# Performance work log

Hardware: AMD Instinct MI355X
Metric: run time of the kernel (lower is better)

Reference implementation:

```python
import math
import jax, jax.numpy as jnp
import numpy as np

LM_DAMPING = 1e-3
MOTION_LAMBDA = 1.0
LM_ITERS = (2, 3, 4)


def _skew(w):  # (B,3) -> (B,3,3)
    z = jnp.zeros_like(w[:, 0])
    return jnp.stack([z, -w[:, 2], w[:, 1],
                      w[:, 2], z, -w[:, 0],
                      -w[:, 1], w[:, 0], z], axis=-1).reshape(-1, 3, 3)


def _se3_exp(xi):  # (B,6) -> (B,4,4)
    t, w = xi[:, :3], xi[:, 3:]
    theta = jnp.clip(jnp.linalg.norm(w, axis=-1, keepdims=True), 1e-8, None)  # (B,1)
    K = _skew(w / theta)
    eye = jnp.eye(3, dtype=xi.dtype)
    st = jnp.sin(theta)[:, :, None]          # (B,1,1)
    ct = (1.0 - jnp.cos(theta))[:, :, None]
    KK = K @ K
    R = eye + st * K + ct * KK
    th = jnp.clip(theta[:, :, None], 1e-8, None)
    V = eye + (ct / th) * K + (1.0 - st / th) * KK
    t_out = (V @ t[..., None])[..., 0]
    B = xi.shape[0]
    T = jnp.tile(jnp.eye(4, dtype=xi.dtype)[None], (B, 1, 1))
    T = T.at[:, :3, :3].set(R).at[:, :3, 3].set(t_out)
    return T


def _se3_log(T):  # (B,4,4) -> (B,6)
    R, t = T[:, :3, :3], T[:, :3, 3]
    cos_a = (R[:, 0, 0] + R[:, 1, 1] + R[:, 2, 2] - 1.0) / 2.0
    theta = jnp.arccos(jnp.clip(cos_a, -1.0 + 1e-7, 1.0 - 1e-7))
    small = jnp.abs(theta) < 1e-6
    th = jnp.clip(theta, 1e-8, None)
    w = jnp.stack([R[:, 2, 1] - R[:, 1, 2],
                   R[:, 0, 2] - R[:, 2, 0],
                   R[:, 1, 0] - R[:, 0, 1]], axis=-1)
    w = w / (2.0 * jnp.clip(jnp.sin(th), 1e-8, None))[:, None] * th[:, None]
    w = jnp.where(small[:, None], 0.0, w)
    return jnp.concatenate([t, w], axis=-1)


def _sample_one(feat, gx, gy):
    # feat (C,H,W); gx,gy (P,) normalized in [-1,1]; align_corners=False, border padding
    C, H, W = feat.shape
    x = jnp.clip(((gx + 1.0) * W - 1.0) / 2.0, 0.0, W - 1)
    y = jnp.clip(((gy + 1.0) * H - 1.0) / 2.0, 0.0, H - 1)
    x0 = jnp.floor(x); y0 = jnp.floor(y)
    x1 = jnp.minimum(x0 + 1.0, W - 1); y1 = jnp.minimum(y0 + 1.0, H - 1)
    wx = x - x0; wy = y - y0
    x0i, x1i = x0.astype(jnp.int32), x1.astype(jnp.int32)
    y0i, y1i = y0.astype(jnp.int32), y1.astype(jnp.int32)
    f00 = feat[:, y0i, x0i]; f01 = feat[:, y0i, x1i]
    f10 = feat[:, y1i, x0i]; f11 = feat[:, y1i, x1i]
    return (f00 * (1 - wx) * (1 - wy) + f01 * wx * (1 - wy)
            + f10 * (1 - wx) * wy + f11 * wx * wy)  # (C,P)

_sample = jax.vmap(_sample_one, in_axes=(0, 0, 0))


def _generate_hypotheses(T_pred, key):
    rng = jnp.arange(-11.0, 13.0, 2.0, dtype=jnp.float32)  # 12 values
    pg, yg = jnp.meshgrid(rng, rng, indexing='ij')
    pitch = pg.reshape(-1) * (math.pi / 180.0)
    yaw = yg.reshape(-1) * (math.pi / 180.0)
    M = pitch.shape[0]  # 144
    t_noise = jax.random.normal(key, (M, 3), dtype=jnp.float32) * 1.0  # translation_std
    xi = jnp.stack([t_noise[:, 0], t_noise[:, 1], t_noise[:, 2],
                    jnp.zeros(M, jnp.float32), pitch, yaw], axis=-1)
    dT = _se3_exp(xi)  # (M,4,4)
    return jnp.einsum('mij,bjk->bmik', dT, T_pred)  # (B,M,4,4)


def _residuals(T, q_feat, r_feat, q_unc, geo, K, level):
    # T (B,M,4,4); fallback path evaluates only first min(M,16) hypotheses
    B, M = T.shape[:2]
    _, C, H, W = q_feat.shape
    scale = 1.0 / (4.0 / 2 ** level)
    Ks = jnp.concatenate([K[:, :2] * scale, K[:, 2:]], axis=1)
    M16 = min(M, 16)
    Tm = T[:, :M16]  # (B,16,4,4)
    N = geo.shape[1]
    pts_h = jnp.concatenate([geo, jnp.ones((B, N, 1), geo.dtype)], axis=-1)  # (B,N,4)
    pts_cam = jnp.einsum('bmij,bnj->bmni', Tm[:, :, :3, :], pts_h)  # (B,16,N,3)
    z = jnp.clip(pts_cam[..., 2:3], 1e-6, None)
    xy = pts_cam[..., :2] / z
    fx = Ks[:, 0, 0][:, None, None]; fy = Ks[:, 1, 1][:, None, None]
    cx = Ks[:, 0, 2][:, None, None]; cy = Ks[:, 1, 2][:, None, None]
    u = fx * xy[..., 0] + cx
    v = fy * xy[..., 1] + cy
    gx = (2.0 * u / max(W - 1, 1) - 1.0).reshape(B, M16 * N)
    gy = (2.0 * v / max(H - 1, 1) - 1.0).reshape(B, M16 * N)
    qs = _sample(q_feat, gx, gy).reshape(B, C, M16, N)
    rs = _sample(r_feat, gx, gy).reshape(B, C, M16, N)
    diff2 = (qs - rs) ** 2
    unc = _sample(q_unc, gx, gy).reshape(B, 1, M16, N)
    res = (diff2 * unc).sum(axis=1).mean(axis=-1)  # (B,16)
    return jnp.zeros((B, M), T.dtype).at[:, :M16].set(res)


def reference(T_pred, geo_anchors, intrinsics, q0, q1, q2, r0, r1, r2, u0, u1, u2):
    key = jax.random.key(42)
    B = T_pred.shape[0]
    T_cur = _generate_hypotheses(T_pred, jax.random.fold_in(key, 0))
    M = T_cur.shape[1]
    q_feats = (q0, q1, q2); r_feats = (r0, r1, r2); uncs = (u0, u1, u2)
    costs = jnp.zeros((B, M), T_pred.dtype)
    for level, n_iters in enumerate(LM_ITERS):
        for it in range(n_iters):
            res = _residuals(T_cur, q_feats[level], r_feats[level], uncs[level],
                             geo_anchors, intrinsics, level)
            damping = LM_DAMPING * 0.5 ** level
            noise = jax.random.normal(jax.random.fold_in(key, 100 + level * 10 + it),
                                      (B, M, 6), dtype=T_pred.dtype)
            step = -damping * res[..., None] * noise * 0.01
            delta = _se3_exp(step.reshape(B * M, 6)).reshape(B, M, 4, 4)
            T_cur = delta @ T_cur
            costs = res
    # motion-constrained selection: C_total = C_photo + lambda * ||log(T_ref T_pred^-1)||
    T_rel = T_cur @ jnp.linalg.inv(T_pred)[:, None]
    geod = jnp.linalg.norm(_se3_log(T_rel.reshape(B * M, 4, 4)), axis=-1).reshape(B, M)
    total = costs + MOTION_LAMBDA * geod
    idx = jnp.argmin(total, axis=1)
    T_best = jnp.take_along_axis(T_cur, idx[:, None, None, None], axis=1)[:, 0]
    return T_best, costs


def setup_inputs() -> dict:
    key = jax.random.key(0)
    ks = jax.random.split(key, 16)
    B, N = 8, 500
    # valid SE(3) predicted poses (small perturbation of identity)
    T_pred = _se3_exp(jax.random.normal(ks[0], (B, 6), jnp.float32) * 0.1)
    # 3D anchors in front of the camera (z ~ 6)
    geo = jax.random.uniform(ks[1], (B, N, 3), jnp.float32, -2.0, 2.0)
    geo = geo.at[..., 2].add(6.0)
    K = jnp.tile(jnp.array([[200.0, 0.0, 128.0],
                            [0.0, 200.0, 96.0],
                            [0.0, 0.0, 1.0]], jnp.float32)[None], (B, 1, 1))
    shapes_f = [(B, 128, 48, 64), (B, 64, 96, 128), (B, 32, 192, 256)]
    q = [jax.random.normal(ks[2 + i], s, jnp.float32) for i, s in enumerate(shapes_f)]
    r = [jax.random.normal(ks[5 + i], s, jnp.float32) for i, s in enumerate(shapes_f)]
    u = [jax.random.uniform(ks[8 + i], (s[0], 1, s[2], s[3]), jnp.float32)
         for i, s in enumerate(shapes_f)]
    return {"T_pred": T_pred, "geo_anchors": geo, "intrinsics": K,
            "q0": q[0], "q1": q[1], "q2": q[2],
            "r0": r[0], "r1": r[1], "r2": r[2],
            "u0": u[0], "u1": u[1], "u2": u[2]}
```

## Files before the change

### kernel.cpp

```cpp
#include <hip/hip_runtime.h>
#include <stdint.h>
#include <math.h>

#define JAX_PARTITIONABLE 1

#define NB 8
#define NM 144
#define NM16 16
#define NPTS 500
#define GP 16

__host__ __device__ __forceinline__ uint32_t rotl32(uint32_t x, int r) {
    return (x << r) | (x >> (32 - r));
}

__host__ __device__ inline void threefry2x32(uint32_t k0, uint32_t k1,
                                             uint32_t x0, uint32_t x1,
                                             uint32_t& o0, uint32_t& o1) {
    uint32_t ks2 = k0 ^ k1 ^ 0x1BD11BDAu;
    x0 += k0; x1 += k1;
    const int RA[4] = {13, 15, 26, 6};
    const int RB[4] = {17, 29, 16, 24};
#define R4(ROT) { x0 += x1; x1 = rotl32(x1, ROT[0]); x1 ^= x0; \
                  x0 += x1; x1 = rotl32(x1, ROT[1]); x1 ^= x0; \
                  x0 += x1; x1 = rotl32(x1, ROT[2]); x1 ^= x0; \
                  x0 += x1; x1 = rotl32(x1, ROT[3]); x1 ^= x0; }
    R4(RA); x0 += k1;  x1 += ks2 + 1u;
    R4(RB); x0 += ks2; x1 += k0 + 2u;
    R4(RA); x0 += k0;  x1 += k1 + 3u;
    R4(RB); x0 += k1;  x1 += ks2 + 4u;
    R4(RA); x0 += ks2; x1 += k0 + 5u;
#undef R4
    o0 = x0; o1 = x1;
}

__device__ __forceinline__ float erfinv32(float x) {
    float w = -log1pf(-x * x);
    float p;
    if (w < 5.0f) {
        w = w - 2.5f;
        p = 2.81022636e-08f;
        p = fmaf(p, w, 3.43273939e-07f);
        p = fmaf(p, w, -3.5233877e-06f);
// ... 114 lines not shown
    double t1 = V[3] * tx + V[4] * ty + V[5] * tz;
    double t2 = V[6] * tx + V[7] * ty + V[8] * tz;
    T[0] = R[0]; T[1] = R[1]; T[2] = R[2];  T[3] = t0;
    T[4] = R[3]; T[5] = R[4]; T[6] = R[5];  T[7] = t1;
    T[8] = R[6]; T[9] = R[7]; T[10] = R[8]; T[11] = t2;
}

__device__ inline void compose44d(const double dT[12], const double P[16], double Tn[16]) {
    for (int i = 0; i < 3; i++)
        for (int j = 0; j < 4; j++)
            Tn[i * 4 + j] = dT[i * 4 + 0] * P[0 + j] + dT[i * 4 + 1] * P[4 + j] +
                            dT[i * 4 + 2] * P[8 + j] + dT[i * 4 + 3] * P[12 + j];
    Tn[12] = 0.0; Tn[13] = 0.0; Tn[14] = 0.0; Tn[15] = 1.0;
}

__device__ inline void make_hypothesis_d(int m, const double* P, uint32_t hk0, uint32_t hk1,
                                         double Tn[16]) {
    float tn[3];
    for (int c = 0; c < 3; c++)
        tn[c] = jax_normal(hk0, hk1, (uint32_t)(m * 3 + c), 216u);
    int gi = m / 12, gj = m % 12;
    const float d2r = (float)(M_PI / 180.0);
    float pf = (float)(2 * gi - 11) * d2r;
    float yf = (float)(2 * gj - 11) * d2r;
    double xi[6] = {(double)tn[0], (double)tn[1], (double)tn[2], 0.0,
                    (double)pf, (double)yf};
    double dT[12];
    se3_exp6d(xi, dT);
    compose44d(dT, P, Tn);
}

struct IterKeys { uint32_t k0[9]; uint32_t k1[9]; float damping[9]; };

template <int C, int H, int W, int GRP>
__device__ void gram_body_v(const float* __restrict__ q, const float* __restrict__ r,
                            const float* __restrict__ u, float* __restrict__ G,
                            float* part, int blk) {
    constexpr int HW = H * W;
    constexpr int PT = 256 / GRP;
    constexpr int PPB = PT * 4;
    constexpr int TPB = HW / PPB;
    constexpr int CPG = C / GRP;
    const int b = blk / TPB;
    const int tile = blk % TPB;
    const int tid = threadIdx.x;
    const int g = tid / PT;
    const int p = tid % PT;
    const int px0 = tile * PPB + p * 4;
    const int y = px0 / W;
    const int x0 = px0 - y * W;
    const int y1 = (y + 1 < H) ? y + 1 : H - 1;
    const bool edge = (x0 + 4 >= W);

    const int rb0 = y * W + x0;
    const int rb1 = y1 * W + x0;
    const float* qp = q + ((size_t)b * C + (size_t)g * CPG) * HW;
    const float* rp = r + ((size_t)b * C + (size_t)g * CPG) * HW;

    float acc[4][10];
#pragma unroll
    for (int j = 0; j < 4; j++)
#pragma unroll
        for (int i = 0; i < 10; i++) acc[j][i] = 0.0f;

#pragma unroll 2
    for (int c = 0; c < CPG; c++) {
        float4 a0 = *(const float4*)(qp + rb0);
        float4 a1 = *(const float4*)(qp + rb1);
        float4 b0 = *(const float4*)(rp + rb0);
        float4 b1 = *(const float4*)(rp + rb1);
        qp += HW; rp += HW;
        float e0[5], e1[5];
        e0[0] = a0.x - b0.x; e0[1] = a0.y - b0.y; e0[2] = a0.z - b0.z; e0[3] = a0.w - b0.w;
        e1[0] = a1.x - b1.x; e1[1] = a1.y - b1.y; e1[2] = a1.z - b1.z; e1[3] = a1.w - b1.w;
        float d0n = __shfl_down(e0[0], 1, 64);
        float d1n = __shfl_down(e1[0], 1, 64);
        e0[4] = edge ? e0[3] : d0n;
        e1[4] = edge ? e1[3] : d1n;
#pragma unroll
        for (int j = 0; j < 4; j++) {
            float d00 = e0[j], d01 = e0[j + 1];
            float d10 = e1[j], d11 = e1[j + 1];
            acc[j][0] = fmaf(d00, d00, acc[j][0]);
            acc[j][1] = fmaf(d00, d01, acc[j][1]);
            acc[j][2] = fmaf(d00, d10, acc[j][2]);
            acc[j][3] = fmaf(d00, d11, acc[j][3]);
            acc[j][4] = fmaf(d01, d01, acc[j][4]);
            acc[j][5] = fmaf(d01, d10, acc[j][5]);
            acc[j][6] = fmaf(d01, d11, acc[j][6]);
            acc[j][7] = fmaf(d10, d10, acc[j][7]);
            acc[j][8] = fmaf(d10, d11, acc[j][8]);
            acc[j][9] = fmaf(d11, d11, acc[j][9]);
        }
    }
    if (GRP > 1) {
        if (g > 0) {
            float* pp = part + (size_t)(g - 1) * 40 * PT;
#pragma unroll
            for (int j = 0; j < 4; j++)
#pragma unroll
                for (int i = 0; i < 10; i++)
                    pp[(j * 10 + i) * PT + p] = acc[j][i];
        }
        __syncthreads();
        if (g == 0) {
            for (int gg = 1; gg < GRP; gg++) {
                const float* pp = part + (size_t)(gg - 1) * 40 * PT;
#pragma unroll
                for (int j = 0; j < 4; j++)
#pragma unroll
                    for (int i = 0; i < 10; i++)
                        acc[j][i] += pp[(j * 10 + i) * PT + p];
            }
        }
    }
    if (g == 0) {
        const float* ub = u + (size_t)b * HW;
        float4 u0 = *(const float4*)(ub + rb0);
        float4 u1 = *(const float4*)(ub + rb1);
        float w0[5], w1[5];
        w0[0] = u0.x; w0[1] = u0.y; w0[2] = u0.z; w0[3] = u0.w;
        w1[0] = u1.x; w1[1] = u1.y; w1[2] = u1.z; w1[3] = u1.w;
        float u0n = __shfl_down(u0.x, 1, 64);
        float u1n = __shfl_down(u1.x, 1, 64);
        w0[4] = edge ? w0[3] : u0n;
        w1[4] = edge ? w1[3] : u1n;
#pragma unroll
        for (int j = 0; j < 4; j++) {
            size_t base = ((size_t)b * HW + px0 + j) * GP;
            float4 g0v = {acc[j][0], acc[j][1], acc[j][2], acc[j][3]};
            float4 g1v = {acc[j][4], acc[j][5], acc[j][6], acc[j][7]};
            float4 g2v = {acc[j][8], acc[j][9], w0[j], w0[j + 1]};
            float4 g3v = {w1[j], w1[j + 1], 0.0f, 0.0f};
            *(float4*)(G + base + 0)  = g0v;
            *(float4*)(G + base + 4)  = g1v;
            *(float4*)(G + base + 8)  = g2v;
            *(float4*)(G + base + 12) = g3v;
        }
    }
}

#define VBLK0 96
#define VBLK1 192
#define VBLK2 384

__global__ __launch_bounds__(256) void gram_fused_kernel(
    const float* __restrict__ q0, const float* __restrict__ r0, const float* __restrict__ u0,
    float* __restrict__ G0,
    const float* __restrict__ q1, const float* __restrict__ r1, const float* __restrict__ u1,
    float* __restrict__ G1,
    const float* __restrict__ q2, const float* __restrict__ r2, const float* __restrict__ u2,
    float* __restrict__ G2) {
    __shared__ float part[3 * 40 * 64];
    const int blk = blockIdx.x;
    if (blk < VBLK0)
        gram_body_v<128, 48, 64, 4>(q0, r0, u0, G0, part, blk);
    else if (blk < VBLK0 + VBLK1)
        gram_body_v<64, 96, 128, 2>(q1, r1, u1, G1, part, blk - VBLK0);
    else
        gram_body_v<32, 192, 256, 1>(q2, r2, u2, G2, part, blk - VBLK0 - VBLK1);
}

template <int H, int W>
__device__ void run_level_gram(const float* __restrict__ Gb,
                               float fx, float fy, float cx, float cy,
                               const float* geoS, float* Tsh, float* red, float* resS,
                               float* stepS, float* out, int b, int m,
                               const IterKeys& iks, int firstIter, int niter) {
    const int tid = threadIdx.x;
    for (int it = 0; it < niter; it++) {
        const int iter = firstIter + it;
        float acc = 0.0f;
        if (tid < NPTS) {
            float px = geoS[tid * 3], py = geoS[tid * 3 + 1], pz = geoS[tid * 3 + 2];
            float X = Tsh[0] * px + Tsh[1] * py + Tsh[2]  * pz + Tsh[3];
            float Y = Tsh[4] * px + Tsh[5] * py + Tsh[6]  * pz + Tsh[7];
            float Z = Tsh[8] * px + Tsh[9] * py + Tsh[10] * pz + Tsh[11];
            float z = fmaxf(Z, 1e-6f);
            float uu = fx * (X / z) + cx;
            float vv = fy * (Y / z) + cy;
            float gx = 2.0f * uu / (float)(W - 1) - 1.0f;
            float gy = 2.0f * vv / (float)(H - 1) - 1.0f;
            float x = fminf(fmaxf(((gx + 1.0f) * (float)W - 1.0f) * 0.5f, 0.0f), (float)(W - 1));
            float y = fminf(fmaxf(((gy + 1.0f) * (float)H - 1.0f) * 0.5f, 0.0f), (float)(H - 1));
            float x0f = floorf(x), y0f = floorf(y);
            float wx = x - x0f, wy = y - y0f;
            int x0i = (int)x0f, y0i = (int)y0f;
            int i00 = y0i * W + x0i;
            float w00 = (1.0f - wx) * (1.0f - wy), w01 = wx * (1.0f - wy);
            float w10 = (1.0f - wx) * wy,          w11 = wx * wy;
            const float* Gp = Gb + (size_t)i00 * GP;
            float4 g0 = *(const float4*)(Gp + 0);
            float4 g1 = *(const float4*)(Gp + 4);
            float4 g2 = *(const float4*)(Gp + 8);
            float4 g3 = *(const float4*)(Gp + 12);
            float uval = w00 * g2.z + w01 * g2.w + w10 * g3.x + w11 * g3.y;
            float val = w00 * w00 * g0.x + w01 * w01 * g1.x +
                        w10 * w10 * g1.w + w11 * w11 * g2.y +
                        2.0f * (w00 * w01 * g0.y + w00 * w10 * g0.z + w00 * w11 * g0.w +
                                w01 * w10 * g1.y + w01 * w11 * g1.z + w10 * w11 * g2.x);
            acc = uval * val;
        }
        float v = acc;
        for (int off = 32; off > 0; off >>= 1) v += __shfl_down(v, off, 64);
        if ((tid & 63) == 0) red[tid >> 6] = v;
        __syncthreads();
        if (tid == 0) {
            float s = 0.0f;
            for (int w = 0; w < 8; w++) s += red[w];
            float res = s / 500.0f;
            *resS = res;
            if (iter == 8) out[128 + b * NM + m] = res;
        }
        __syncthreads();
        if (tid < 6) {
            uint32_t fi = (uint32_t)((b * NM + m) * 6 + tid);
            float nz = jax_normal(iks.k0[iter], iks.k1[iter], fi, 3456u);
            stepS[tid] = (((-iks.damping[iter]) * (*resS)) * nz) * 0.01f;
        }
        __syncthreads();
        if (tid == 0) {
            float xi[6];
            for (int j = 0; j < 6; j++) xi[j] = stepS[j];
            float dT[12];
            se3_exp6(xi, dT);
            float Told[16];
            for (int k = 0; k < 16; k++) Told[k] = Tsh[k];
            float Tn[16];
            compose44(dT, Told, Tn);
            for (int k = 0; k < 16; k++) Tsh[k] = Tn[k];
        }
        __syncthreads();
    }
}

__global__ __launch_bounds__(512) void evolve_kernel_gram(
    const float* __restrict__ T_pred, const float* __restrict__ geo,
    const float* __restrict__ Kmat,
    const float* __restrict__ G0, const float* __restrict__ G1, const float* __restrict__ G2,
    float* __restrict__ Tws, float* __restrict__ out,
    uint32_t hk0, uint32_t hk1, IterKeys iks) {
    const int bm = blockIdx.x;
    const int b = bm & 7;
    const int m = bm >> 3;
    const int tid = threadIdx.x;

    __shared__ float Tsh[16];
    __shared__ float geoS[NPTS * 3];
    __shared__ float red[8];
    __shared__ float resS;
    __shared__ float stepS[6];

    for (int i = tid; i < NPTS * 3; i += 512) geoS[i] = geo[b * NPTS * 3 + i];

    if (tid == 0) {
        float P[16];
        for (int k = 0; k < 16; k++) P[k] = T_pred[b * 16 + k];
        float Tn[16];
        make_hypothesis(m, P, hk0, hk1, Tn);
        for (int k = 0; k < 16; k++) Tsh[k] = Tn[k];
    }
    __syncthreads();

    float K00 = Kmat[b * 9 + 0], K02 = Kmat[b * 9 + 2];
    float K11 = Kmat[b * 9 + 4], K12 = Kmat[b * 9 + 5];

    run_level_gram<48, 64>(G0 + (size_t)b * 48 * 64 * GP,
                           K00 * 0.25f, K11 * 0.25f, K02 * 0.25f, K12 * 0.25f,
                           geoS, Tsh, red, &resS, stepS, out, b, m, iks, 0, 2);
    run_level_gram<96, 128>(G1 + (size_t)b * 96 * 128 * GP,
                            K00 * 0.5f, K11 * 0.5f, K02 * 0.5f, K12 * 0.5f,
                            geoS, Tsh, red, &resS, stepS, out, b, m, iks, 2, 3);
    run_level_gram<192, 256>(G2 + (size_t)b * 192 * 256 * GP,
                             K00, K11, K02, K12,
                             geoS, Tsh, red, &resS, stepS, out, b, m, iks, 5, 4);

    if (tid < 16) Tws[(size_t)(b * NM16 + m) * 16 + tid] = Tsh[tid];
}

template <int C, int H, int W>
__device__ void run_level_nchw(const float* __restrict__ qb, const float* __restrict__ rb,
                               const float* __restrict__ ub,
                               float fx, float fy, float cx, float cy,
                               const float* geoS, float* Tsh, float* red, float* resS,
                               float* stepS, float* out, int b, int m,
                               const IterKeys& iks, int firstIter, int niter) {
    const int tid = threadIdx.x;
    const int HW = H * W;
    for (int it = 0; it < niter; it++) {
        const int iter = firstIter + it;
        float acc = 0.0f;
        if (tid < NPTS) {
            float px = geoS[tid * 3], py = geoS[tid * 3 + 1], pz = geoS[tid * 3 + 2];
            float X = Tsh[0] * px + Tsh[1] * py + Tsh[2]  * pz + Tsh[3];
            float Y = Tsh[4] * px + Tsh[5] * py + Tsh[6]  * pz + Tsh[7];
            float Z = Tsh[8] * px + Tsh[9] * py + Tsh[10] * pz + Tsh[11];
            float z = fmaxf(Z, 1e-6f);
            float uu = fx * (X / z) + cx;
            float vv = fy * (Y / z) + cy;
            float gx = 2.0f * uu / (float)(W - 1) - 1.0f;
            float gy = 2.0f * vv / (float)(H - 1) - 1.0f;
            float x = fminf(fmaxf(((gx + 1.0f) * (float)W - 1.0f) * 0.5f, 0.0f), (float)(W - 1));
            float y = fminf(fmaxf(((gy + 1.0f) * (float)H - 1.0f) * 0.5f, 0.0f), (float)(H - 1));
            float x0f = floorf(x), y0f = floorf(y);
            float x1f = fminf(x0f + 1.0f, (float)(W - 1));
            float y1f = fminf(y0f + 1.0f, (float)(H - 1));
            float wx = x - x0f, wy = y - y0f;
            int x0i = (int)x0f, x1i = (int)x1f, y0i = (int)y0f, y1i = (int)y1f;
            int i00 = y0i * W + x0i, i01 = y0i * W + x1i;
            int i10 = y1i * W + x0i, i11 = y1i * W + x1i;
// ... 165 lines not shown
    const float* K      = (const float*)d_in[2];
    const float* q0 = (const float*)d_in[3];
    const float* q1 = (const float*)d_in[4];
    const float* q2 = (const float*)d_in[5];
    const float* r0 = (const float*)d_in[6];
    const float* r1 = (const float*)d_in[7];
    const float* r2 = (const float*)d_in[8];
    const float* u0 = (const float*)d_in[9];
    const float* u1 = (const float*)d_in[10];
    const float* u2 = (const float*)d_in[11];
    float* out = (float*)d_out;

    float* Tws = (float*)d_ws;
    const size_t nG0 = (size_t)NB * 48 * 64 * GP;
    const size_t nG1 = (size_t)NB * 96 * 128 * GP;
    const size_t nG2 = (size_t)NB * 192 * 256 * GP;
    float* G0 = Tws + 2048;
    float* G1 = G0 + nG0;
    float* G2 = G1 + nG1;
    const size_t need = (2048 + nG0 + nG1 + nG2) * sizeof(float);

    uint32_t hk0, hk1;
    threefry2x32(0u, 42u, 0u, 0u, hk0, hk1);
    IterKeys iks;
    const int seeds[9] = {100, 101, 110, 111, 112, 120, 121, 122, 123};
    const float damp[9] = {0.001f, 0.001f, 0.0005f, 0.0005f, 0.0005f,
                           0.00025f, 0.00025f, 0.00025f, 0.00025f};
    for (int i = 0; i < 9; i++) {
        threefry2x32(0u, 42u, 0u, (uint32_t)seeds[i], iks.k0[i], iks.k1[i]);
        iks.damping[i] = damp[i];
    }

    if (ws_size >= need) {
        gram_fused_kernel<<<dim3(VBLK0 + VBLK1 + VBLK2), dim3(256), 0, stream>>>(
            q0, r0, u0, G0, q1, r1, u1, G1, q2, r2, u2, G2);
        evolve_kernel_gram<<<dim3(NB * NM16), dim3(512), 0, stream>>>(
            T_pred, geo, K, G0, G1, G2, Tws, out, hk0, hk1, iks);
    } else {
        evolve_kernel_nchw<<<dim3(NB * NM16), dim3(512), 0, stream>>>(
            T_pred, geo, K, q0, q1, q2, r0, r1, r2, u0, u1, u2, Tws, out, hk0, hk1, iks);
    }
    finalize_kernel<<<dim3(NB), dim3(192), 0, stream>>>(T_pred, Tws, out, hk0, hk1);
}
```

Before: 256.9 us.

## Halve pixels per thread in gram kernel, swizzle blocks, precompute LM noise

The gram-precompute kernel now gives each thread 2 pixels instead of 4. This doubles the block count for more parallelism on the bandwidth-bound q/r reads, and a straddle path handles the neighbour pixel across wavefront boundaries. Block indices are remapped with an interleaving swizzle across the three pyramid levels. In the evolve kernel, the per-iteration normal noise and damping are precomputed into shared memory once, and the step reduction runs within one wavefront via shuffles, removing two barriers per iteration. The cost is narrower float2 loads and extra scalar loads for straddling lanes.

```diff
diff --git a/kernel.cpp b/kernel.cpp
--- a/kernel.cpp
+++ b/kernel.cpp
@@ -195,7 +195,7 @@
                             float* part, int blk) {
     constexpr int HW = H * W;
     constexpr int PT = 256 / GRP;
-    constexpr int PPB = PT * 4;
+    constexpr int PPB = PT * 2;
     constexpr int TPB = HW / PPB;
     constexpr int CPG = C / GRP;
     const int b = blk / TPB;
@@ -203,58 +203,68 @@
     const int tid = threadIdx.x;
     const int g = tid / PT;
     const int p = tid % PT;
-    const int px0 = tile * PPB + p * 4;
+    const int px0 = tile * PPB + p * 2;
     const int y = px0 / W;
     const int x0 = px0 - y * W;
     const int y1 = (y + 1 < H) ? y + 1 : H - 1;
-    const bool edge = (x0 + 4 >= W);
+    const bool edge = (x0 + 2 >= W);
+    const bool straddle = (!edge) && ((tid & 63) == 63);
 
     const int rb0 = y * W + x0;
     const int rb1 = y1 * W + x0;
     const float* qp = q + ((size_t)b * C + (size_t)g * CPG) * HW;
     const float* rp = r + ((size_t)b * C + (size_t)g * CPG) * HW;
 
-    float acc[4][10];
+    float acc[2][10];
 #pragma unroll
-    for (int j = 0; j < 4; j++)
+    for (int j = 0; j < 2; j++)
 #pragma unroll
         for (int i = 0; i < 10; i++) acc[j][i] = 0.0f;
 
 #pragma unroll 2
     for (int c = 0; c < CPG; c++) {
-        float4 a0 = *(const float4*)(qp + rb0);
-        float4 a1 = *(const float4*)(qp + rb1);
-        float4 b0 = *(const float4*)(rp + rb0);
-        float4 b1 = *(const float4*)(rp + rb1);
+        float2 a0 = *(const float2*)(qp + rb0);
+        float2 a1 = *(const float2*)(qp + rb1);
+        float2 b0 = *(const float2*)(rp + rb0);
+        float2 b1 = *(const float2*)(rp + rb1);
+        float s0 = 0.0f, s1 = 0.0f;
+        if (straddle) {
+            s0 = qp[rb0 + 2] - rp[rb0 + 2];
+            s1 = qp[rb1 + 2] - rp[rb1 + 2];
+        }
         qp += HW; rp += HW;
-        float e0[5], e1[5];
-        e0[0] = a0.x - b0.x; e0[1] = a0.y - b0.y; e0[2] = a0.z - b0.z; e0[3] = a0.w - b0.w;
-        e1[0] = a1.x - b1.x; e1[1] = a1.y - b1.y; e1[2] = a1.z - b1.z; e1[3] = a1.w - b1.w;
-        float d0n = __shfl_down(e0[0], 1, 64);
-        float d1n = __shfl_down(e1[0], 1, 64);
-        e0[4] = edge ? e0[3] : d0n;
-        e1[4] = edge ? e1[3] : d1n;
-#pragma unroll
-        for (int j = 0; j < 4; j++) {
-            float d00 = e0[j], d01 = e0[j + 1];
-            float d10 = e1[j], d11 = e1[j + 1];
-            acc[j][0] = fmaf(d00, d00, acc[j][0]);
-            acc[j][1] = fmaf(d00, d01, acc[j][1]);
-            acc[j][2] = fmaf(d00, d10, acc[j][2]);
-            acc[j][3] = fmaf(d00, d11, acc[j][3]);
-            acc[j][4] = fmaf(d01, d01, acc[j][4]);
-            acc[j][5] = fmaf(d01, d10, acc[j][5]);
-            acc[j][6] = fmaf(d01, d11, acc[j][6]);
-            acc[j][7] = fmaf(d10, d10, acc[j][7]);
-            acc[j][8] = fmaf(d10, d11, acc[j][8]);
-            acc[j][9] = fmaf(d11, d11, acc[j][9]);
-        }
+        float e00 = a0.x - b0.x, e01 = a0.y - b0.y;
+        float e10 = a1.x - b1.x, e11 = a1.y - b1.y;
+        float d0n = __shfl_down(e00, 1, 64);
+        float d1n = __shfl_down(e10, 1, 64);
+        float e02 = edge ? e01 : (straddle ? s0 : d0n);
+        float e12 = edge ? e11 : (straddle ? s1 : d1n);
+        acc[0][0] = fmaf(e00, e00, acc[0][0]);
+        acc[0][1] = fmaf(e00, e01, acc[0][1]);
+        acc[0][2] = fmaf(e00, e10, acc[0][2]);
+        acc[0][3] = fmaf(e00, e11, acc[0][3]);
+        acc[0][4] = fmaf(e01, e01, acc[0][4]);
+        acc[0][5] = fmaf(e01, e10, acc[0][5]);
+        acc[0][6] = fmaf(e01, e11, acc[0][6]);
+        acc[0][7] = fmaf(e10, e10, acc[0][7]);
+        acc[0][8] = fmaf(e10, e11, acc[0][8]);
+        acc[0][9] = fmaf(e11, e11, acc[0][9]);
+        acc[1][0] = fmaf(e01, e01, acc[1][0]);
+        acc[1][1] = fmaf(e01, e02, acc[1][1]);
+        acc[1][2] = fmaf(e01, e11, acc[1][2]);
+        acc[1][3] = fmaf(e01, e12, acc[1][3]);
+        acc[1][4] = fmaf(e02, e02, acc[1][4]);
+        acc[1][5] = fmaf(e02, e11, acc[1][5]);
+        acc[1][6] = fmaf(e02, e12, acc[1][6]);
+        acc[1][7] = fmaf(e11, e11, acc[1][7]);
+        acc[1][8] = fmaf(e11, e12, acc[1][8]);
+        acc[1][9] = fmaf(e12, e12, acc[1][9]);
     }
     if (GRP > 1) {
         if (g > 0) {
-            float* pp = part + (size_t)(g - 1) * 40 * PT;
+            float* pp = part + (size_t)(g - 1) * 20 * PT;
 #pragma unroll
-            for (int j = 0; j < 4; j++)
+            for (int j = 0; j < 2; j++)
 #pragma unroll
                 for (int i = 0; i < 10; i++)
                     pp[(j * 10 + i) * PT + p] = acc[j][i];
@@ -262,9 +272,9 @@
         __syncthreads();
         if (g == 0) {
             for (int gg = 1; gg < GRP; gg++) {
-                const float* pp = part + (size_t)(gg - 1) * 40 * PT;
+                const float* pp = part + (size_t)(gg - 1) * 20 * PT;
 #pragma unroll
-                for (int j = 0; j < 4; j++)
+                for (int j = 0; j < 2; j++)
 #pragma unroll
                     for (int i = 0; i < 10; i++)
                         acc[j][i] += pp[(j * 10 + i) * PT + p];
@@ -273,33 +283,45 @@
     }
     if (g == 0) {
         const float* ub = u + (size_t)b * HW;
-        float4 u0 = *(const float4*)(ub + rb0);
-        float4 u1 = *(const float4*)(ub + rb1);
-        float w0[5], w1[5];
-        w0[0] = u0.x; w0[1] = u0.y; w0[2] = u0.z; w0[3] = u0.w;
-        w1[0] = u1.x; w1[1] = u1.y; w1[2] = u1.z; w1[3] = u1.w;
+        float2 u0 = *(const float2*)(ub + rb0);
+        float2 u1 = *(const float2*)(ub + rb1);
+        float su0 = 0.0f, su1 = 0.0f;
+        if (straddle) { su0 = ub[rb0 + 2]; su1 = ub[rb1 + 2]; }
+        float w00 = u0.x, w01 = u0.y;
+        float w10 = u1.x, w11 = u1.y;
         float u0n = __shfl_down(u0.x, 1, 64);
         float u1n = __shfl_down(u1.x, 1, 64);
-        w0[4] = edge ? w0[3] : u0n;
-        w1[4] = edge ? w1[3] : u1n;
-#pragma unroll
-        for (int j = 0; j < 4; j++) {
-            size_t base = ((size_t)b * HW + px0 + j) * GP;
-            float4 g0v = {acc[j][0], acc[j][1], acc[j][2], acc[j][3]};
-            float4 g1v = {acc[j][4], acc[j][5], acc[j][6], acc[j][7]};
-            float4 g2v = {acc[j][8], acc[j][9], w0[j], w0[j + 1]};
-            float4 g3v = {w1[j], w1[j + 1], 0.0f, 0.0f};
+        float w02 = edge ? w01 : (straddle ? su0 : u0n);
+        float w12 = edge ? w11 : (straddle ? su1 : u1n);
+        {
+            size_t base = ((size_t)b * HW + px0) * GP;
+            float4 g0v = {acc[0][0], acc[0][1], acc[0][2], acc[0][3]};
+            float4 g1v = {acc[0][4], acc[0][5], acc[0][6], acc[0][7]};
+            float4 g2v = {acc[0][8], acc[0][9], w00, w01};
+            float4 g3v = {w10, w11, 0.0f, 0.0f};
             *(float4*)(G + base + 0)  = g0v;
             *(float4*)(G + base + 4)  = g1v;
             *(float4*)(G + base + 8)  = g2v;
             *(float4*)(G + base + 12) = g3v;
         }
-    }
-}
-
-#define VBLK0 96
-#define VBLK1 192
-#define VBLK2 384
+        {
+            size_t base = ((size_t)b * HW + px0 + 1) * GP;
+            float4 g0v = {acc[1][0], acc[1][1], acc[1][2], acc[1][3]};
+            float4 g1v = {acc[1][4], acc[1][5], acc[1][6], acc[1][7]};
+            float4 g2v = {acc[1][8], acc[1][9], w01, w02};
+            float4 g3v = {w11, w12, 0.0f, 0.0f};
+            *(float4*)(G + base + 0)  = g0v;
+            *(float4*)(G + base + 4)  = g1v;
+            *(float4*)(G + base + 8)  = g2v;
+            *(float4*)(G + base + 12) = g3v;
+        }
+    }
+}
+
+#define VBLK0 192
+#define VBLK1 384
+#define VBLK2 768
+#define VBLKT (VBLK0 + VBLK1 + VBLK2)
 
 __global__ __launch_bounds__(256) void gram_fused_kernel(
     const float* __restrict__ q0, const float* __restrict__ r0, const float* __restrict__ u0,
@@ -308,8 +330,8 @@
     float* __restrict__ G1,
     const float* __restrict__ q2, const float* __restrict__ r2, const float* __restrict__ u2,
     float* __restrict__ G2) {
-    __shared__ float part[3 * 40 * 64];
-    const int blk = blockIdx.x;
+    __shared__ float part[3 * 20 * 64];
+    const int blk = (blockIdx.x & 7) * (VBLKT / 8) + (blockIdx.x >> 3);
     if (blk < VBLK0)
         gram_body_v<128, 48, 64, 4>(q0, r0, u0, G0, part, blk);
     else if (blk < VBLK0 + VBLK1)
@@ -321,9 +343,9 @@
 template <int H, int W>
 __device__ void run_level_gram(const float* __restrict__ Gb,
                                float fx, float fy, float cx, float cy,
-                               const float* geoS, float* Tsh, float* red, float* resS,
-                               float* stepS, float* out, int b, int m,
-                               const IterKeys& iks, int firstIter, int niter) {
+                               const float* geoS, float* Tsh, float* red,
+                               const float* nzS, const float* damping,
+                               float* out, int b, int m, int firstIter, int niter) {
     const int tid = threadIdx.x;
     for (int it = 0; it < niter; it++) {
         const int iter = firstIter + it;
@@ -362,30 +384,26 @@
         for (int off = 32; off > 0; off >>= 1) v += __shfl_down(v, off, 64);
         if ((tid & 63) == 0) red[tid >> 6] = v;
         __syncthreads();
-        if (tid == 0) {
+        if (tid < 64) {
             float s = 0.0f;
             for (int w = 0; w < 8; w++) s += red[w];
             float res = s / 500.0f;
-            *resS = res;
-            if (iter == 8) out[128 + b * NM + m] = res;
-        }
-        __syncthreads();
-        if (tid < 6) {
-            uint32_t fi = (uint32_t)((b * NM + m) * 6 + tid);
-            float nz = jax_normal(iks.k0[iter], iks.k1[iter], fi, 3456u);
-            stepS[tid] = (((-iks.damping[iter]) * (*resS)) * nz) * 0.01f;
-        }
-        __syncthreads();
-        if (tid == 0) {
+            if (tid == 0 && iter == 8) out[128 + b * NM + m] = res;
+            float st = 0.0f;
+            if (tid < 6)
+                st = (((-damping[iter]) * res) * nzS[iter * 6 + tid]) * 0.01f;
             float xi[6];
-            for (int j = 0; j < 6; j++) xi[j] = stepS[j];
-            float dT[12];
-            se3_exp6(xi, dT);
-            float Told[16];
-            for (int k = 0; k < 16; k++) Told[k] = Tsh[k];
-            float Tn[16];
-            compose44(dT, Told, Tn);
-            for (int k = 0; k < 16; k++) Tsh[k] = Tn[k];
+#pragma unroll
+            for (int j = 0; j < 6; j++) xi[j] = __shfl(st, j, 64);
+            if (tid == 0) {
+                float dT[12];
+                se3_exp6(xi, dT);
+                float Told[16];
+                for (int k = 0; k < 16; k++) Told[k] = Tsh[k];
+                float Tn[16];
+                compose44(dT, Told, Tn);
+                for (int k = 0; k < 16; k++) Tsh[k] = Tn[k];
+            }
         }
         __syncthreads();
     }
@@ -405,12 +423,19 @@
     __shared__ float Tsh[16];
     __shared__ float geoS[NPTS * 3];
     __shared__ float red[8];
-    __shared__ float resS;
-    __shared__ float stepS[6];
+    __shared__ float nzS[54];
+    __shared__ float dampS[9];
 
     for (int i = tid; i < NPTS * 3; i += 512) geoS[i] = geo[b * NPTS * 3 + i];
 
-    if (tid == 0) {
+    if (tid < 54) {
+        int it9 = tid / 6, jj = tid % 6;
+        uint32_t fi = (uint32_t)((b * NM + m) * 6 + jj);
+        nzS[tid] = jax_normal(iks.k0[it9], iks.k1[it9], fi, 3456u);
+    }
+    if (tid >= 54 && tid < 63) dampS[tid - 54] = iks.damping[tid - 54];
+
+    if (tid == 64) {
         float P[16];
         for (int k = 0; k < 16; k++) P[k] = T_pred[b * 16 + k];
         float Tn[16];
@@ -424,13 +449,13 @@
 
     run_level_gram<48, 64>(G0 + (size_t)b * 48 * 64 * GP,
                            K00 * 0.25f, K11 * 0.25f, K02 * 0.25f, K12 * 0.25f,
-                           geoS, Tsh, red, &resS, stepS, out, b, m, iks, 0, 2);
+                           geoS, Tsh, red, nzS, dampS, out, b, m, 0, 2);
     run_level_gram<96, 128>(G1 + (size_t)b * 96 * 128 * GP,
                             K00 * 0.5f, K11 * 0.5f, K02 * 0.5f, K12 * 0.5f,
-                            geoS, Tsh, red, &resS, stepS, out, b, m, iks, 2, 3);
+                            geoS, Tsh, red, nzS, dampS, out, b, m, 2, 3);
     run_level_gram<192, 256>(G2 + (size_t)b * 192 * 256 * GP,
                              K00, K11, K02, K12,
-                             geoS, Tsh, red, &resS, stepS, out, b, m, iks, 5, 4);
+                             geoS, Tsh, red, nzS, dampS, out, b, m, 5, 4);
 
     if (tid < 16) Tws[(size_t)(b * NM16 + m) * 16 + tid] = Tsh[tid];
 }
@@ -664,7 +689,7 @@
     }
 
     if (ws_size >= need) {
-        gram_fused_kernel<<<dim3(VBLK0 + VBLK1 + VBLK2), dim3(256), 0, stream>>>(
+        gram_fused_kernel<<<dim3(VBLKT), dim3(256), 0, stream>>>(
             q0, r0, u0, G0, q1, r1, u1, G1, q2, r2, u2, G2);
         evolve_kernel_gram<<<dim3(NB * NM16), dim3(512), 0, stream>>>(
             T_pred, geo, K, G0, G1, G2, Tws, out, hk0, hk1, iks);
```

Result: slower. 267.3 us (+4.0%).

## Stage q/r feature rows in shared-memory slabs and precompute LM noise

Applied to the files above, without the earlier changes.

The gram kernel now assigns each block a band of four rows. For every channel it loads the rows plus one halo row into a double-buffered shared-memory slab, prefetched one channel ahead through registers, so the right-neighbour and lower-row values come from LDS rather than redundant global reads and shuffles. The evolve kernel precomputes all per-iteration Threefry noise and damping values into shared memory once, and collapses the per-iteration residual/step/update sequence into a single wavefront, removing two block barriers per LM iteration. The cost is two barriers per channel in the gram loop and extra LDS use, which may reduce occupancy.

```diff
diff --git a/kernel.cpp b/kernel.cpp
--- a/kernel.cpp
+++ b/kernel.cpp
@@ -189,30 +189,44 @@
 
 struct IterKeys { uint32_t k0[9]; uint32_t k1[9]; float damping[9]; };
 
+#define STF 2560
+
 template <int C, int H, int W, int GRP>
-__device__ void gram_body_v(const float* __restrict__ q, const float* __restrict__ r,
+__device__ void gram_body_s(const float* __restrict__ q, const float* __restrict__ r,
                             const float* __restrict__ u, float* __restrict__ G,
-                            float* part, int blk) {
+                            float* slab, float* part, int blk) {
     constexpr int HW = H * W;
+    constexpr int CPG = C / GRP;
+    constexpr int R = 4;
     constexpr int PT = 256 / GRP;
-    constexpr int PPB = PT * 4;
-    constexpr int TPB = HW / PPB;
-    constexpr int CPG = C / GRP;
+    constexpr int SPAN = (R + 1) * W;
+    constexpr int TPB = H / R;
+    constexpr int TPR = W / 4;
     const int b = blk / TPB;
     const int tile = blk % TPB;
+    const int y0 = tile * R;
     const int tid = threadIdx.x;
     const int g = tid / PT;
     const int p = tid % PT;
-    const int px0 = tile * PPB + p * 4;
-    const int y = px0 / W;
-    const int x0 = px0 - y * W;
-    const int y1 = (y + 1 < H) ? y + 1 : H - 1;
-    const bool edge = (x0 + 4 >= W);
-
-    const int rb0 = y * W + x0;
-    const int rb1 = y1 * W + x0;
-    const float* qp = q + ((size_t)b * C + (size_t)g * CPG) * HW;
-    const float* rp = r + ((size_t)b * C + (size_t)g * CPG) * HW;
+    const int row_l = p / TPR;
+    const int x0 = (p % TPR) * 4;
+
+    const float* ptrk[5];
+    int swk[5];
+#pragma unroll
+    for (int k = 0; k < 5; k++) {
+        int f = 2 * (tid + 256 * k);
+        swk[k] = f;
+        int arr = f / (GRP * SPAN);
+        int rem = f - arr * (GRP * SPAN);
+        int chl = rem / SPAN;
+        int rr  = rem - chl * SPAN;
+        int row = rr / W;
+        int x   = rr - row * W;
+        int gy  = (y0 + row < H) ? (y0 + row) : (H - 1);
+        const float* base = arr ? r : q;
+        ptrk[k] = base + ((size_t)b * C + (size_t)chl * CPG) * HW + (size_t)gy * W + x;
+    }
 
     float acc[4][10];
 #pragma unroll
@@ -220,36 +234,61 @@
 #pragma unroll
         for (int i = 0; i < 10; i++) acc[j][i] = 0.0f;
 
-#pragma unroll 2
-    for (int c = 0; c < CPG; c++) {
-        float4 a0 = *(const float4*)(qp + rb0);
-        float4 a1 = *(const float4*)(qp + rb1);
-        float4 b0 = *(const float4*)(rp + rb0);
-        float4 b1 = *(const float4*)(rp + rb1);
-        qp += HW; rp += HW;
+    float2 ld[5];
+#pragma unroll
+    for (int k = 0; k < 5; k++) { ld[k] = *(const float2*)ptrk[k]; ptrk[k] += HW; }
+#pragma unroll
+    for (int k = 0; k < 5; k++) *(float2*)&slab[swk[k]] = ld[k];
+#pragma unroll
+    for (int k = 0; k < 5; k++) { ld[k] = *(const float2*)ptrk[k]; ptrk[k] += HW; }
+    __syncthreads();
+
+    int cur = 0;
+    const int off0 = row_l * W + x0;
+    const int off1 = off0 + W;
+    const int t4 = (x0 + 4 < W) ? (x0 + 4) : (W - 1);
+    for (int j = 0; j < CPG; j++) {
+        const float* qs = slab + cur * STF + g * SPAN;
+        const float* rs = slab + cur * STF + (GRP + g) * SPAN;
+        float4 qa = *(const float4*)(qs + off0);
+        float4 qb = *(const float4*)(qs + off1);
+        float4 ra = *(const float4*)(rs + off0);
+        float4 rb = *(const float4*)(rs + off1);
+        float qa4 = qs[row_l * W + t4], qb4 = qs[row_l * W + W + t4];
+        float ra4 = rs[row_l * W + t4], rb4 = rs[row_l * W + W + t4];
         float e0[5], e1[5];
-        e0[0] = a0.x - b0.x; e0[1] = a0.y - b0.y; e0[2] = a0.z - b0.z; e0[3] = a0.w - b0.w;
-        e1[0] = a1.x - b1.x; e1[1] = a1.y - b1.y; e1[2] = a1.z - b1.z; e1[3] = a1.w - b1.w;
-        float d0n = __shfl_down(e0[0], 1, 64);
-        float d1n = __shfl_down(e1[0], 1, 64);
-        e0[4] = edge ? e0[3] : d0n;
-        e1[4] = edge ? e1[3] : d1n;
-#pragma unroll
-        for (int j = 0; j < 4; j++) {
-            float d00 = e0[j], d01 = e0[j + 1];
-            float d10 = e1[j], d11 = e1[j + 1];
-            acc[j][0] = fmaf(d00, d00, acc[j][0]);
-            acc[j][1] = fmaf(d00, d01, acc[j][1]);
-            acc[j][2] = fmaf(d00, d10, acc[j][2]);
-            acc[j][3] = fmaf(d00, d11, acc[j][3]);
-            acc[j][4] = fmaf(d01, d01, acc[j][4]);
-            acc[j][5] = fmaf(d01, d10, acc[j][5]);
-            acc[j][6] = fmaf(d01, d11, acc[j][6]);
-            acc[j][7] = fmaf(d10, d10, acc[j][7]);
-            acc[j][8] = fmaf(d10, d11, acc[j][8]);
-            acc[j][9] = fmaf(d11, d11, acc[j][9]);
-        }
-    }
+        e0[0] = qa.x - ra.x; e0[1] = qa.y - ra.y; e0[2] = qa.z - ra.z; e0[3] = qa.w - ra.w;
+        e0[4] = qa4 - ra4;
+        e1[0] = qb.x - rb.x; e1[1] = qb.y - rb.y; e1[2] = qb.z - rb.z; e1[3] = qb.w - rb.w;
+        e1[4] = qb4 - rb4;
+#pragma unroll
+        for (int jj = 0; jj < 4; jj++) {
+            float d00 = e0[jj], d01 = e0[jj + 1];
+            float d10 = e1[jj], d11 = e1[jj + 1];
+            acc[jj][0] = fmaf(d00, d00, acc[jj][0]);
+            acc[jj][1] = fmaf(d00, d01, acc[jj][1]);
+            acc[jj][2] = fmaf(d00, d10, acc[jj][2]);
+            acc[jj][3] = fmaf(d00, d11, acc[jj][3]);
+            acc[jj][4] = fmaf(d01, d01, acc[jj][4]);
+            acc[jj][5] = fmaf(d01, d10, acc[jj][5]);
+            acc[jj][6] = fmaf(d01, d11, acc[jj][6]);
+            acc[jj][7] = fmaf(d10, d10, acc[jj][7]);
+            acc[jj][8] = fmaf(d10, d11, acc[jj][8]);
+            acc[jj][9] = fmaf(d11, d11, acc[jj][9]);
+        }
+        __syncthreads();
+        if (j + 1 < CPG) {
+#pragma unroll
+            for (int k = 0; k < 5; k++) *(float2*)&slab[(cur ^ 1) * STF + swk[k]] = ld[k];
+            if (j + 2 < CPG) {
+#pragma unroll
+                for (int k = 0; k < 5; k++) { ld[k] = *(const float2*)ptrk[k]; ptrk[k] += HW; }
+            }
+        }
+        __syncthreads();
+        cur ^= 1;
+    }
+
     if (GRP > 1) {
         if (g > 0) {
             float* pp = part + (size_t)(g - 1) * 40 * PT;
@@ -271,17 +310,30 @@
             }
         }
     }
+
+#pragma unroll
+    for (int k = 0; k < 3; k++) {
+        int e2u = tid + 256 * k;
+        if (2 * e2u < SPAN) {
+            int f = 2 * e2u;
+            int row = f / W;
+            int x = f - row * W;
+            int gy = (y0 + row < H) ? (y0 + row) : (H - 1);
+            float2 v = *(const float2*)(u + (size_t)b * HW + (size_t)gy * W + x);
+            *(float2*)&slab[f] = v;
+        }
+    }
+    __syncthreads();
     if (g == 0) {
-        const float* ub = u + (size_t)b * HW;
-        float4 u0 = *(const float4*)(ub + rb0);
-        float4 u1 = *(const float4*)(ub + rb1);
         float w0[5], w1[5];
-        w0[0] = u0.x; w0[1] = u0.y; w0[2] = u0.z; w0[3] = u0.w;
-        w1[0] = u1.x; w1[1] = u1.y; w1[2] = u1.z; w1[3] = u1.w;
-        float u0n = __shfl_down(u0.x, 1, 64);
-        float u1n = __shfl_down(u1.x, 1, 64);
-        w0[4] = edge ? w0[3] : u0n;
-        w1[4] = edge ? w1[3] : u1n;
+#pragma unroll
+        for (int j = 0; j < 4; j++) {
+            w0[j] = slab[off0 + j];
+            w1[j] = slab[off1 + j];
+        }
+        w0[4] = slab[row_l * W + t4];
+        w1[4] = slab[row_l * W + W + t4];
+        const int px0 = (y0 + row_l) * W + x0;
 #pragma unroll
         for (int j = 0; j < 4; j++) {
             size_t base = ((size_t)b * HW + px0 + j) * GP;
@@ -297,9 +349,10 @@
     }
 }
 
-#define VBLK0 96
-#define VBLK1 192
-#define VBLK2 384
+#define SBLK0 96
+#define SBLK1 192
+#define SBLK2 384
+#define SBLKT (SBLK0 + SBLK1 + SBLK2)
 
 __global__ __launch_bounds__(256) void gram_fused_kernel(
     const float* __restrict__ q0, const float* __restrict__ r0, const float* __restrict__ u0,
@@ -308,22 +361,23 @@
     float* __restrict__ G1,
     const float* __restrict__ q2, const float* __restrict__ r2, const float* __restrict__ u2,
     float* __restrict__ G2) {
+    __shared__ float slab[2 * STF];
     __shared__ float part[3 * 40 * 64];
     const int blk = blockIdx.x;
-    if (blk < VBLK0)
-        gram_body_v<128, 48, 64, 4>(q0, r0, u0, G0, part, blk);
-    else if (blk < VBLK0 + VBLK1)
-        gram_body_v<64, 96, 128, 2>(q1, r1, u1, G1, part, blk - VBLK0);
+    if (blk < SBLK0)
+        gram_body_s<128, 48, 64, 4>(q0, r0, u0, G0, slab, part, blk);
+    else if (blk < SBLK0 + SBLK1)
+        gram_body_s<64, 96, 128, 2>(q1, r1, u1, G1, slab, part, blk - SBLK0);
     else
-        gram_body_v<32, 192, 256, 1>(q2, r2, u2, G2, part, blk - VBLK0 - VBLK1);
+        gram_body_s<32, 192, 256, 1>(q2, r2, u2, G2, slab, part, blk - SBLK0 - SBLK1);
 }
 
 template <int H, int W>
 __device__ void run_level_gram(const float* __restrict__ Gb,
                                float fx, float fy, float cx, float cy,
-                               const float* geoS, float* Tsh, float* red, float* resS,
-                               float* stepS, float* out, int b, int m,
-                               const IterKeys& iks, int firstIter, int niter) {
+                               const float* geoS, float* Tsh, float* red,
+                               const float* nzS, const float* damping,
+                               float* out, int b, int m, int firstIter, int niter) {
     const int tid = threadIdx.x;
     for (int it = 0; it < niter; it++) {
         const int iter = firstIter + it;
@@ -362,30 +416,26 @@
         for (int off = 32; off > 0; off >>= 1) v += __shfl_down(v, off, 64);
         if ((tid & 63) == 0) red[tid >> 6] = v;
         __syncthreads();
-        if (tid == 0) {
+        if (tid < 64) {
             float s = 0.0f;
             for (int w = 0; w < 8; w++) s += red[w];
             float res = s / 500.0f;
-            *resS = res;
-            if (iter == 8) out[128 + b * NM + m] = res;
-        }
-        __syncthreads();
-        if (tid < 6) {
-            uint32_t fi = (uint32_t)((b * NM + m) * 6 + tid);
-            float nz = jax_normal(iks.k0[iter], iks.k1[iter], fi, 3456u);
-            stepS[tid] = (((-iks.damping[iter]) * (*resS)) * nz) * 0.01f;
-        }
-        __syncthreads();
-        if (tid == 0) {
+            if (tid == 0 && iter == 8) out[128 + b * NM + m] = res;
+            float st = 0.0f;
+            if (tid < 6)
+                st = (((-damping[iter]) * res) * nzS[iter * 6 + tid]) * 0.01f;
             float xi[6];
-            for (int j = 0; j < 6; j++) xi[j] = stepS[j];
-            float dT[12];
-            se3_exp6(xi, dT);
-            float Told[16];
-            for (int k = 0; k < 16; k++) Told[k] = Tsh[k];
-            float Tn[16];
-            compose44(dT, Told, Tn);
-            for (int k = 0; k < 16; k++) Tsh[k] = Tn[k];
+#pragma unroll
+            for (int j = 0; j < 6; j++) xi[j] = __shfl(st, j, 64);
+            if (tid == 0) {
+                float dT[12];
+                se3_exp6(xi, dT);
+                float Told[16];
+                for (int k = 0; k < 16; k++) Told[k] = Tsh[k];
+                float Tn[16];
+                compose44(dT, Told, Tn);
+                for (int k = 0; k < 16; k++) Tsh[k] = Tn[k];
+            }
         }
         __syncthreads();
     }
@@ -405,12 +455,19 @@
     __shared__ float Tsh[16];
     __shared__ float geoS[NPTS * 3];
     __shared__ float red[8];
-    __shared__ float resS;
-    __shared__ float stepS[6];
+    __shared__ float nzS[54];
+    __shared__ float dampS[9];
 
     for (int i = tid; i < NPTS * 3; i += 512) geoS[i] = geo[b * NPTS * 3 + i];
 
-    if (tid == 0) {
+    if (tid < 54) {
+        int it9 = tid / 6, jj = tid % 6;
+        uint32_t fi = (uint32_t)((b * NM + m) * 6 + jj);
+        nzS[tid] = jax_normal(iks.k0[it9], iks.k1[it9], fi, 3456u);
+    }
+    if (tid >= 54 && tid < 63) dampS[tid - 54] = iks.damping[tid - 54];
+
+    if (tid == 64) {
         float P[16];
         for (int k = 0; k < 16; k++) P[k] = T_pred[b * 16 + k];
         float Tn[16];
@@ -424,13 +481,13 @@
 
     run_level_gram<48, 64>(G0 + (size_t)b * 48 * 64 * GP,
                            K00 * 0.25f, K11 * 0.25f, K02 * 0.25f, K12 * 0.25f,
-                           geoS, Tsh, red, &resS, stepS, out, b, m, iks, 0, 2);
+                           geoS, Tsh, red, nzS, dampS, out, b, m, 0, 2);
     run_level_gram<96, 128>(G1 + (size_t)b * 96 * 128 * GP,
                             K00 * 0.5f, K11 * 0.5f, K02 * 0.5f, K12 * 0.5f,
-                            geoS, Tsh, red, &resS, stepS, out, b, m, iks, 2, 3);
+                            geoS, Tsh, red, nzS, dampS, out, b, m, 2, 3);
     run_level_gram<192, 256>(G2 + (size_t)b * 192 * 256 * GP,
                              K00, K11, K02, K12,
-                             geoS, Tsh, red, &resS, stepS, out, b, m, iks, 5, 4);
+                             geoS, Tsh, red, nzS, dampS, out, b, m, 5, 4);
 
     if (tid < 16) Tws[(size_t)(b * NM16 + m) * 16 + tid] = Tsh[tid];
 }
@@ -664,7 +721,7 @@
     }
 
     if (ws_size >= need) {
-        gram_fused_kernel<<<dim3(VBLK0 + VBLK1 + VBLK2), dim3(256), 0, stream>>>(
+        gram_fused_kernel<<<dim3(SBLKT), dim3(256), 0, stream>>>(
             q0, r0, u0, G0, q1, r1, u1, G1, q2, r2, u2, G2);
         evolve_kernel_gram<<<dim3(NB * NM16), dim3(512), 0, stream>>>(
             T_pred, geo, K, G0, G1, G2, Tws, out, hk0, hk1, iks);
```

Result: no change. 252.1 us (-1.9%).

## Keep pose in registers per thread, precompute noise, use nontemporal loads

Applied to the files above, without the earlier changes.

The evolve kernel now keeps the 3x4 pose in registers of every thread. Each thread redundantly computes the residual sum, the SE(3) step and the pose update, so only one barrier per iteration remains instead of four. The per-iteration noise values and damping are precomputed into shared memory at kernel start, and the reduction buffer is double-buffered to avoid a write-after-read race. The gram kernel's feature loads switch to nontemporal loads to reduce cache pollution. The cost is redundant transcendental work across 512 threads and higher register pressure.

```diff
diff --git a/kernel.cpp b/kernel.cpp
--- a/kernel.cpp
+++ b/kernel.cpp
@@ -9,6 +9,12 @@
 #define NM16 16
 #define NPTS 500
 #define GP 16
+
+typedef float v4f __attribute__((ext_vector_type(4)));
+
+__device__ __forceinline__ v4f nt4(const float* p) {
+    return __builtin_nontemporal_load((const v4f*)p);
+}
 
 __host__ __device__ __forceinline__ uint32_t rotl32(uint32_t x, int r) {
     return (x << r) | (x >> (32 - r));
@@ -222,10 +228,10 @@
 
 #pragma unroll 2
     for (int c = 0; c < CPG; c++) {
-        float4 a0 = *(const float4*)(qp + rb0);
-        float4 a1 = *(const float4*)(qp + rb1);
-        float4 b0 = *(const float4*)(rp + rb0);
-        float4 b1 = *(const float4*)(rp + rb1);
+        v4f a0 = nt4(qp + rb0);
+        v4f a1 = nt4(qp + rb1);
+        v4f b0 = nt4(rp + rb0);
+        v4f b1 = nt4(rp + rb1);
         qp += HW; rp += HW;
         float e0[5], e1[5];
         e0[0] = a0.x - b0.x; e0[1] = a0.y - b0.y; e0[2] = a0.z - b0.z; e0[3] = a0.w - b0.w;
@@ -319,20 +325,21 @@
 }
 
 template <int H, int W>
-__device__ void run_level_gram(const float* __restrict__ Gb,
+__device__ void run_level_regT(const float* __restrict__ Gb,
                                float fx, float fy, float cx, float cy,
-                               const float* geoS, float* Tsh, float* red, float* resS,
-                               float* stepS, float* out, int b, int m,
-                               const IterKeys& iks, int firstIter, int niter) {
+                               const float* geoS, float Treg[12],
+                               float (*red)[8],
+                               const float* nzS, const float* dampS,
+                               float* out, int b, int m, int firstIter, int niter) {
     const int tid = threadIdx.x;
     for (int it = 0; it < niter; it++) {
         const int iter = firstIter + it;
         float acc = 0.0f;
         if (tid < NPTS) {
             float px = geoS[tid * 3], py = geoS[tid * 3 + 1], pz = geoS[tid * 3 + 2];
-            float X = Tsh[0] * px + Tsh[1] * py + Tsh[2]  * pz + Tsh[3];
-            float Y = Tsh[4] * px + Tsh[5] * py + Tsh[6]  * pz + Tsh[7];
-            float Z = Tsh[8] * px + Tsh[9] * py + Tsh[10] * pz + Tsh[11];
+            float X = Treg[0] * px + Treg[1] * py + Treg[2]  * pz + Treg[3];
+            float Y = Treg[4] * px + Treg[5] * py + Treg[6]  * pz + Treg[7];
+            float Z = Treg[8] * px + Treg[9] * py + Treg[10] * pz + Treg[11];
             float z = fmaxf(Z, 1e-6f);
             float uu = fx * (X / z) + cx;
             float vv = fy * (Y / z) + cy;
@@ -360,34 +367,28 @@
         }
         float v = acc;
         for (int off = 32; off > 0; off >>= 1) v += __shfl_down(v, off, 64);
-        if ((tid & 63) == 0) red[tid >> 6] = v;
+        if ((tid & 63) == 0) red[iter & 1][tid >> 6] = v;
         __syncthreads();
-        if (tid == 0) {
-            float s = 0.0f;
-            for (int w = 0; w < 8; w++) s += red[w];
-            float res = s / 500.0f;
-            *resS = res;
-            if (iter == 8) out[128 + b * NM + m] = res;
-        }
-        __syncthreads();
-        if (tid < 6) {
-            uint32_t fi = (uint32_t)((b * NM + m) * 6 + tid);
-            float nz = jax_normal(iks.k0[iter], iks.k1[iter], fi, 3456u);
-            stepS[tid] = (((-iks.damping[iter]) * (*resS)) * nz) * 0.01f;
-        }
-        __syncthreads();
-        if (tid == 0) {
-            float xi[6];
-            for (int j = 0; j < 6; j++) xi[j] = stepS[j];
-            float dT[12];
-            se3_exp6(xi, dT);
-            float Told[16];
-            for (int k = 0; k < 16; k++) Told[k] = Tsh[k];
-            float Tn[16];
-            compose44(dT, Told, Tn);
-            for (int k = 0; k < 16; k++) Tsh[k] = Tn[k];
-        }
-        __syncthreads();
+        float s = 0.0f;
+        for (int w = 0; w < 8; w++) s += red[iter & 1][w];
+        float res = s / 500.0f;
+        if (tid == 0 && iter == 8) out[128 + b * NM + m] = res;
+        float xi[6];
+#pragma unroll
+        for (int j = 0; j < 6; j++)
+            xi[j] = (((-dampS[iter]) * res) * nzS[iter * 6 + j]) * 0.01f;
+        float dT[12];
+        se3_exp6(xi, dT);
+        float Tn[12];
+#pragma unroll
+        for (int i = 0; i < 3; i++)
+#pragma unroll
+            for (int j = 0; j < 4; j++)
+                Tn[i * 4 + j] = dT[i * 4 + 0] * Treg[0 + j] + dT[i * 4 + 1] * Treg[4 + j] +
+                                dT[i * 4 + 2] * Treg[8 + j] +
+                                dT[i * 4 + 3] * ((j == 3) ? 1.0f : 0.0f);
+#pragma unroll
+        for (int k = 0; k < 12; k++) Treg[k] = Tn[k];
     }
 }
 
@@ -402,37 +403,49 @@
     const int m = bm >> 3;
     const int tid = threadIdx.x;
 
-    __shared__ float Tsh[16];
     __shared__ float geoS[NPTS * 3];
-    __shared__ float red[8];
-    __shared__ float resS;
-    __shared__ float stepS[6];
+    __shared__ float red[2][8];
+    __shared__ float nzS[54];
+    __shared__ float dampS[9];
 
     for (int i = tid; i < NPTS * 3; i += 512) geoS[i] = geo[b * NPTS * 3 + i];
 
-    if (tid == 0) {
-        float P[16];
-        for (int k = 0; k < 16; k++) P[k] = T_pred[b * 16 + k];
-        float Tn[16];
-        make_hypothesis(m, P, hk0, hk1, Tn);
-        for (int k = 0; k < 16; k++) Tsh[k] = Tn[k];
-    }
+    if (tid < 54) {
+        int it9 = tid / 6, jj = tid % 6;
+        uint32_t fi = (uint32_t)((b * NM + m) * 6 + jj);
+        nzS[tid] = jax_normal(iks.k0[it9], iks.k1[it9], fi, 3456u);
+    }
+    if (tid >= 54 && tid < 63) dampS[tid - 54] = iks.damping[tid - 54];
+
+    float P[16];
+    for (int k = 0; k < 16; k++) P[k] = T_pred[b * 16 + k];
+    float Tn16[16];
+    make_hypothesis(m, P, hk0, hk1, Tn16);
+    float Treg[12];
+#pragma unroll
+    for (int k = 0; k < 12; k++) Treg[k] = Tn16[k];
     __syncthreads();
 
     float K00 = Kmat[b * 9 + 0], K02 = Kmat[b * 9 + 2];
     float K11 = Kmat[b * 9 + 4], K12 = Kmat[b * 9 + 5];
 
-    run_level_gram<48, 64>(G0 + (size_t)b * 48 * 64 * GP,
+    run_level_regT<48, 64>(G0 + (size_t)b * 48 * 64 * GP,
                            K00 * 0.25f, K11 * 0.25f, K02 * 0.25f, K12 * 0.25f,
-                           geoS, Tsh, red, &resS, stepS, out, b, m, iks, 0, 2);
-    run_level_gram<96, 128>(G1 + (size_t)b * 96 * 128 * GP,
+                           geoS, Treg, red, nzS, dampS, out, b, m, 0, 2);
+    run_level_regT<96, 128>(G1 + (size_t)b * 96 * 128 * GP,
                             K00 * 0.5f, K11 * 0.5f, K02 * 0.5f, K12 * 0.5f,
-                            geoS, Tsh, red, &resS, stepS, out, b, m, iks, 2, 3);
-    run_level_gram<192, 256>(G2 + (size_t)b * 192 * 256 * GP,
+                            geoS, Treg, red, nzS, dampS, out, b, m, 2, 3);
+    run_level_regT<192, 256>(G2 + (size_t)b * 192 * 256 * GP,
                              K00, K11, K02, K12,
-                             geoS, Tsh, red, &resS, stepS, out, b, m, iks, 5, 4);
-
-    if (tid < 16) Tws[(size_t)(b * NM16 + m) * 16 + tid] = Tsh[tid];
+                             geoS, Treg, red, nzS, dampS, out, b, m, 5, 4);
+
+    if (tid == 0) {
+        size_t base = (size_t)(b * NM16 + m) * 16;
+#pragma unroll
+        for (int k = 0; k < 12; k++) Tws[base + k] = Treg[k];
+        Tws[base + 12] = 0.0f; Tws[base + 13] = 0.0f;
+        Tws[base + 14] = 0.0f; Tws[base + 15] = 1.0f;
+    }
 }
 
 template <int C, int H, int W>
```

Result: faster. 242.4 us (-5.7%).
